# Kernel tuning notes

Hardware: AMD Instinct MI355X
Metric: run time of the kernel (lower is better)

## Reference

```python
import jax, jax.numpy as jnp
import numpy as np

C = 512  # channels
B, S = 8, 2048


def setup_inputs() -> dict:
    key = jax.random.key(0)
    ks = jax.random.split(key, 8)
    x = jax.random.normal(ks[0], (B, S, C), dtype=jnp.float32)
    eigenvalues = jax.random.normal(ks[1], (B, S), dtype=jnp.float32)
    init = 1.0 / np.sqrt(C)
    Wq = jax.random.normal(ks[2], (C, C), dtype=jnp.float32) * init
    bq = jnp.zeros((C,), dtype=jnp.float32)
    Wk = jax.random.normal(ks[3], (C, C), dtype=jnp.float32) * init
    bk = jnp.zeros((C,), dtype=jnp.float32)
    Wv = jax.random.normal(ks[4], (C, C), dtype=jnp.float32) * init
    bv = jnp.zeros((C,), dtype=jnp.float32)
    return {"x": x, "eigenvalues": eigenvalues, "Wq": Wq, "bq": bq,
            "Wk": Wk, "bk": bk, "Wv": Wv, "bv": bv}


def reference(x, eigenvalues, Wq, bq, Wk, bk, Wv, bv):
    # torch nn.Linear: y = x @ W^T + b
    scale = 1.0 / np.sqrt(x.shape[-1])
    Q = jnp.einsum('bsc,dc->bsd', x, Wq) + bq
    K = jnp.einsum('bsc,dc->bsd', x, Wk) + bk
    V = jnp.einsum('bsc,dc->bsd', x, Wv) + bv
    # scores: [B, S(query), S(key)]
    scores = jnp.einsum('bqd,bkd->bqk', Q, K) * scale
    eigen_weight = jax.nn.sigmoid(eigenvalues)          # [B, S]
    scores = scores * eigen_weight[:, None, :]          # scale per key position
    attn = jax.nn.softmax(scores, axis=-1)
    return jnp.einsum('bqk,bkd->bqd', attn, V)
```

## Files before the change

kernel.cpp:

```cpp
#include <hip/hip_runtime.h>

typedef unsigned short u16;
using bf16x8 = __attribute__((ext_vector_type(8))) short;
using f32x4  = __attribute__((ext_vector_type(4))) float;

__device__ __forceinline__ u16 f2b(float f) {
    __bf16 h = (__bf16)f;
    return __builtin_bit_cast(unsigned short, h);
}
__device__ __forceinline__ float b2f(u16 u) {
    return (float)__builtin_bit_cast(__bf16, u);
}

__device__ __forceinline__ void gload16(const void* g, void* l) {
    __builtin_amdgcn_global_load_lds(
        (const __attribute__((address_space(1))) unsigned int*)g,
        (__attribute__((address_space(3))) unsigned int*)l, 16, 0, 0);
}

template<int MODE>
__global__ __launch_bounds__(256)
void gemm_bt(const u16* __restrict__ A, const u16* __restrict__ B,
             void* __restrict__ Cv, const float* __restrict__ aux,
             float* __restrict__ rowsum,
             int K, int lda, int ldb, int ldc,
             long strA, long strB, long strC, long strAux, long strRS)
{
    __shared__ __align__(16) u16 sA[128 * 64];
    __shared__ __align__(16) u16 sB[128 * 64];

    const int tid  = threadIdx.x;
    const int lane = tid & 63;
    const int wave = tid >> 6;
    const int wm = wave >> 1, wn = wave & 1;
    const int bn0 = blockIdx.x * 128;
    const int bm0 = blockIdx.y * 128;
    const long z  = blockIdx.z;

    const u16* Ab = A + z * strA;
    const u16* Bb = B + z * strB;
    const float* auxp = aux + z * strAux;

    f32x4 acc[4][4] = {};

    const int l16 = lane & 15;
    const int lk8 = (lane >> 4) * 8;

    for (int k0 = 0; k0 < K; k0 += 64) {
#pragma unroll
        for (int i = 0; i < 4; ++i) {
            const int c   = i * 256 + tid;
            const int row = c >> 3;
            const int kc  = (c & 7) ^ (row & 7);
            const int ldsoff = (i * 256 + wave * 64) * 8;
            gload16(Ab + (long)(bm0 + row) * lda + k0 + kc * 8, &sA[ldsoff]);
            gload16(Bb + (long)(bn0 + row) * ldb + k0 + kc * 8, &sB[ldsoff]);
        }
        __syncthreads();
#pragma unroll
        for (int kk = 0; kk < 64; kk += 32) {
            bf16x8 af[4], bg[4];
#pragma unroll
            for (int m = 0; m < 4; ++m) {
                const int row = wm * 64 + m * 16 + l16;
                int byte_off = row * 128 + (kk + lk8) * 2;
                byte_off ^= (row & 7) << 4;
                af[m] = *(const bf16x8*)((const char*)sA + byte_off);
            }
#pragma unroll
            for (int n = 0; n < 4; ++n) {
                const int row = wn * 64 + n * 16 + l16;
                int byte_off = row * 128 + (kk + lk8) * 2;
                byte_off ^= (row & 7) << 4;
                bg[n] = *(const bf16x8*)((const char*)sB + byte_off);
            }
#pragma unroll
            for (int m = 0; m < 4; ++m)
#pragma unroll
                for (int n = 0; n < 4; ++n)
                    acc[m][n] = __builtin_amdgcn_mfma_f32_16x16x32_bf16(
                        af[m], bg[n], acc[m][n], 0, 0, 0);
        }
        __syncthreads();
    }

    const int rg    = lane >> 4;
    const int orow0 = bm0 + wm * 64;
    const int ocol0 = bn0 + wn * 64;

    if constexpr (MODE == 0) {
        u16* Co = (u16*)Cv + z * strC;
        float bias[4];
#pragma unroll
        for (int n = 0; n < 4; ++n) bias[n] = auxp[ocol0 + n * 16 + l16];
#pragma unroll
        for (int m = 0; m < 4; ++m)
#pragma unroll
            for (int n = 0; n < 4; ++n) {
                const int col = ocol0 + n * 16 + l16;
#pragma unroll
                for (int r = 0; r < 4; ++r) {
                    const int row = orow0 + m * 16 + rg * 4 + r;
                    Co[(long)row * ldc + col] = f2b(acc[m][n][r] + bias[n]);
                }
            }
    } else if constexpr (MODE == 2) {
        u16* Co = (u16*)Cv + z * strC;
        float* rsp = rowsum + z * strRS;
        float wkn[4];
#pragma unroll
        for (int n = 0; n < 4; ++n) wkn[n] = auxp[ocol0 + n * 16 + l16];
#pragma unroll
        for (int m = 0; m < 4; ++m)
#pragma unroll
            for (int r = 0; r < 4; ++r) {
                const int row = orow0 + m * 16 + rg * 4 + r;
                float partial = 0.f;
#pragma unroll
                for (int n = 0; n < 4; ++n) {
                    const int col = ocol0 + n * 16 + l16;
                    const float p = exp2f(acc[m][n][r] * wkn[n]);
                    const u16 pb = f2b(p);
                    Co[(long)row * ldc + col] = pb;
                    partial += b2f(pb);
                }
                partial += __shfl_xor(partial, 1);
                partial += __shfl_xor(partial, 2);
                partial += __shfl_xor(partial, 4);
                partial += __shfl_xor(partial, 8);
                if (l16 == 0) atomicAdd(&rsp[row], partial);
            }
    } else {
        float* Co = (float*)Cv + z * strC;
#pragma unroll
        for (int m = 0; m < 4; ++m)
#pragma unroll
            for (int r = 0; r < 4; ++r) {
                const int row = orow0 + m * 16 + rg * 4 + r;
                const float inv = 1.0f / auxp[row];
#pragma unroll
                for (int n = 0; n < 4; ++n) {
                    const int col = ocol0 + n * 16 + l16;
                    Co[(long)row * ldc + col] = acc[m][n][r] * inv;
                }
            }
    }
}

__global__ void cvt_bf16(const float* __restrict__ in, u16* __restrict__ out, int n4) {
    const int i = blockIdx.x * 256 + threadIdx.x;
    if (i >= n4) return;
    const float4 f = ((const float4*)in)[i];
    ushort4 o;
    o.x = f2b(f.x); o.y = f2b(f.y); o.z = f2b(f.z); o.w = f2b(f.w);
    ((ushort4*)out)[i] = o;
}

__global__ void wk_kernel(const float* __restrict__ eig, float* __restrict__ wk, int n) {
    const int i = blockIdx.x * 256 + threadIdx.x;
    if (i >= n) return;
    const float s = 1.0f / (1.0f + expf(-eig[i]));
    wk[i] = s * (float)(1.4426950408889634 / 22.627416997969522);
}

__global__ __launch_bounds__(256)
void transpose_v(const u16* __restrict__ V, u16* __restrict__ Vt) {
    __shared__ u16 t[64][65];
    const int tid = threadIdx.x;
    const int d0  = blockIdx.x * 64;
    const int bs0 = blockIdx.y * 64;
#pragma unroll
    for (int i = 0; i < 16; ++i) {
        const int idx = i * 256 + tid;
        const int r = idx >> 6, c = idx & 63;
        t[r][c] = V[(long)(bs0 + r) * 512 + d0 + c];
    }
    __syncthreads();
    const long b = bs0 >> 11;
    const int s0 = bs0 & 2047;
#pragma unroll
    for (int i = 0; i < 16; ++i) {
        const int idx = i * 256 + tid;
        const int dch = idx >> 6, s = idx & 63;
        Vt[(b * 512 + d0 + dch) * 2048 + s0 + s] = t[s][dch];
    }
}

extern "C" void kernel_launch(void* const* d_in, const int* in_sizes, int n_in,
                              void* d_out, int out_size, void* d_ws, size_t ws_size,
                              hipStream_t stream) {
    const float* x  = (const float*)d_in[0];
    const float* ev = (const float*)d_in[1];
    const float* Wq = (const float*)d_in[2];
    const float* bq = (const float*)d_in[3];
    const float* Wk = (const float*)d_in[4];
    const float* bk = (const float*)d_in[5];
    const float* Wv = (const float*)d_in[6];
    const float* bv = (const float*)d_in[7];
    float* out = (float*)d_out;

    char* ws = (char*)d_ws;
    u16*   xb     = (u16*)(ws);
    u16*   qkv    = (u16*)(ws + (16ul << 20));
    u16*   Vt     = (u16*)(ws + (64ul << 20));
    u16*   Wb     = (u16*)(ws + (80ul << 20));
    float* biasb  = (float*)(ws + (82ul << 20));
    float* wk     = (float*)(ws + (83ul << 20));
    float* rowsum = (float*)(ws + (84ul << 20));
    u16*   P      = (u16*)(ws + (85ul << 20));

    cvt_bf16<<<dim3(8192), dim3(256), 0, stream>>>(x, xb, 2097152);
    cvt_bf16<<<dim3(256),  dim3(256), 0, stream>>>(Wq, Wb,          65536);
    cvt_bf16<<<dim3(256),  dim3(256), 0, stream>>>(Wk, Wb + 262144, 65536);
    cvt_bf16<<<dim3(256),  dim3(256), 0, stream>>>(Wv, Wb + 524288, 65536);
    hipMemcpyAsync(biasb,        bq, 512 * 4, hipMemcpyDeviceToDevice, stream);
    hipMemcpyAsync(biasb + 512,  bk, 512 * 4, hipMemcpyDeviceToDevice, stream);
    hipMemcpyAsync(biasb + 1024, bv, 512 * 4, hipMemcpyDeviceToDevice, stream);
    wk_kernel<<<dim3(64), dim3(256), 0, stream>>>(ev, wk, 16384);
    hipMemsetAsync(rowsum, 0, 16384 * 4, stream);

    gemm_bt<0><<<dim3(4, 128, 3), dim3(256), 0, stream>>>(
        xb, Wb, qkv, biasb, nullptr,
        512, 512, 512, 512,
        0L, 262144L, 8388608L, 512L, 0L);

    transpose_v<<<dim3(8, 256), dim3(256), 0, stream>>>(qkv + 2 * 8388608L, Vt);

    gemm_bt<2><<<dim3(16, 16, 8), dim3(256), 0, stream>>>(
        qkv, qkv + 8388608L, P, wk, rowsum,
        512, 512, 512, 2048,
        1048576L, 1048576L, 4194304L, 2048L, 2048L);

    gemm_bt<3><<<dim3(4, 16, 8), dim3(256), 0, stream>>>(
        P, Vt, out, rowsum, nullptr,
        2048, 2048, 2048, 512,
        4194304L, 1048576L, 1048576L, 2048L, 0L);
}
```

Measured before the change: 265.3 us.

## Rewrite GEMMs as 8-wave 256-row tiles with double-buffered LDS pipeline

Replaces the 128x128 single-buffered GEMM with an 8-wave kernel using 256-row tiles (256x128 or 256x256), split-K-half double-buffered LDS staging, and hand-placed waitcnt/barriers with setprio around MFMA bursts. It also remaps block indices for L2 locality and fuses the QKV projection into one interleaved 1536-wide output GEMM. The aim is to overlap global-to-LDS loads with MFMA work and raise data reuse per tile. The cost is more registers and LDS, fewer blocks for the PV GEMM, and fragile manual synchronisation.

```diff
diff --git a/kernel.cpp b/kernel.cpp
--- a/kernel.cpp
+++ b/kernel.cpp
@@ -11,115 +11,197 @@
 __device__ __forceinline__ float b2f(u16 u) {
     return (float)__builtin_bit_cast(__bf16, u);
 }
-
-__device__ __forceinline__ void gload16(const void* g, void* l) {
+__device__ __forceinline__ void gload16(const u16* g, const u16* l) {
     __builtin_amdgcn_global_load_lds(
         (const __attribute__((address_space(1))) unsigned int*)g,
         (__attribute__((address_space(3))) unsigned int*)l, 16, 0, 0);
 }
-
-template<int MODE>
-__global__ __launch_bounds__(256)
-void gemm_bt(const u16* __restrict__ A, const u16* __restrict__ B,
-             void* __restrict__ Cv, const float* __restrict__ aux,
-             float* __restrict__ rowsum,
-             int K, int lda, int ldb, int ldc,
-             long strA, long strB, long strC, long strAux, long strRS)
+__device__ __forceinline__ int swz(int row, int q) { return q ^ ((row ^ (row >> 2)) & 3); }
+
+template<int MODE, int NBLK>
+__global__ __launch_bounds__(512, 2)
+void gemm8(const u16* __restrict__ A, const u16* __restrict__ B,
+           void* __restrict__ Cv, const float* __restrict__ aux,
+           float* __restrict__ rowsum,
+           int K, int lda, int ldb, int ldc,
+           long strA, long strB, long strC, long strAux, long strRS)
 {
-    __shared__ __align__(16) u16 sA[128 * 64];
-    __shared__ __align__(16) u16 sB[128 * 64];
+    constexpr int BR  = NBLK * 64;
+    constexpr int VMC = (NBLK == 4) ? 6 : 5;
+    __shared__ __align__(16) u16 sA[2][2][256 * 32];
+    __shared__ __align__(16) u16 sB[2][2][BR * 32];
 
     const int tid  = threadIdx.x;
     const int lane = tid & 63;
     const int wave = tid >> 6;
-    const int wm = wave >> 1, wn = wave & 1;
-    const int bn0 = blockIdx.x * 128;
-    const int bm0 = blockIdx.y * 128;
-    const long z  = blockIdx.z;
-
-    const u16* Ab = A + z * strA;
-    const u16* Bb = B + z * strB;
+    const int wm = wave >> 2, wn = wave & 3;
+    const int l16 = lane & 15, qld = lane >> 4;
+
+    const int gx = gridDim.x, gy = gridDim.y;
+    const int nxy = gx * gy;
+    int li = blockIdx.y * gx + blockIdx.x;
+    li = (li & 7) * (nxy >> 3) + (li >> 3);
+    const int bx = li % gx, by = li / gx;
+    const int bn0 = bx * BR, bm0 = by * 256;
+    const long z = blockIdx.z;
+
+    const u16* Ab = A + z * strA + (long)bm0 * lda;
+    const u16* Bb = B + z * strB + (long)bn0 * ldb;
     const float* auxp = aux + z * strAux;
 
-    f32x4 acc[4][4] = {};
-
-    const int l16 = lane & 15;
-    const int lk8 = (lane >> 4) * 8;
-
-    for (int k0 = 0; k0 < K; k0 += 64) {
-#pragma unroll
-        for (int i = 0; i < 4; ++i) {
-            const int c   = i * 256 + tid;
-            const int row = c >> 3;
-            const int kc  = (c & 7) ^ (row & 7);
-            const int ldsoff = (i * 256 + wave * 64) * 8;
-            gload16(Ab + (long)(bm0 + row) * lda + k0 + kc * 8, &sA[ldsoff]);
-            gload16(Bb + (long)(bn0 + row) * ldb + k0 + kc * 8, &sB[ldsoff]);
-        }
-        __syncthreads();
-#pragma unroll
-        for (int kk = 0; kk < 64; kk += 32) {
-            bf16x8 af[4], bg[4];
-#pragma unroll
-            for (int m = 0; m < 4; ++m) {
-                const int row = wm * 64 + m * 16 + l16;
-                int byte_off = row * 128 + (kk + lk8) * 2;
-                byte_off ^= (row & 7) << 4;
-                af[m] = *(const bf16x8*)((const char*)sA + byte_off);
-            }
-#pragma unroll
-            for (int n = 0; n < 4; ++n) {
-                const int row = wn * 64 + n * 16 + l16;
-                int byte_off = row * 128 + (kk + lk8) * 2;
-                byte_off ^= (row & 7) << 4;
-                bg[n] = *(const bf16x8*)((const char*)sB + byte_off);
-            }
-#pragma unroll
-            for (int m = 0; m < 4; ++m)
-#pragma unroll
-                for (int n = 0; n < 4; ++n)
-                    acc[m][n] = __builtin_amdgcn_mfma_f32_16x16x32_bf16(
-                        af[m], bg[n], acc[m][n], 0, 0, 0);
-        }
-        __syncthreads();
-    }
-
-    const int rg    = lane >> 4;
-    const int orow0 = bm0 + wm * 64;
-    const int ocol0 = bn0 + wn * 64;
+    const int cA0 = tid, cA1 = 512 + tid;
+    const u16* srcA0 = Ab + (long)(cA0 >> 2) * lda + swz(cA0 >> 2, cA0 & 3) * 8;
+    const u16* srcA1 = Ab + (long)(cA1 >> 2) * lda + swz(cA1 >> 2, cA1 & 3) * 8;
+    const int cB1 = (NBLK == 4) ? cA1 : cA0;
+    const u16* srcB0 = Bb + (long)(cA0 >> 2) * ldb + swz(cA0 >> 2, cA0 & 3) * 8;
+    const u16* srcB1 = Bb + (long)(cB1 >> 2) * ldb + swz(cB1 >> 2, cB1 & 3) * 8;
+    const int wch = (tid & ~63) * 8;
+
+#define STAGE_A(sl, kh, colb) do { \
+    gload16(srcA0 + (colb), &sA[sl][kh][wch]); \
+    gload16(srcA1 + (colb), &sA[sl][kh][wch + 4096]); } while (0)
+#define STAGE_B(sl, kh, colb) do { \
+    gload16(srcB0 + (colb), &sB[sl][kh][wch]); \
+    if constexpr (NBLK == 4) { gload16(srcB1 + (colb), &sB[sl][kh][wch + 4096]); } } while (0)
+
+    int offA[8], offB[NBLK];
+#pragma unroll
+    for (int mf = 0; mf < 8; ++mf) {
+        const int row = wm * 128 + mf * 16 + l16;
+        offA[mf] = row * 32 + swz(row, qld) * 8;
+    }
+#pragma unroll
+    for (int n = 0; n < NBLK; ++n) {
+        const int row = wn * (NBLK * 16) + n * 16 + l16;
+        offB[n] = row * 32 + swz(row, qld) * 8;
+    }
+
+    f32x4 acc[8][NBLK] = {};
+    const int NT = K >> 6;
+
+    STAGE_A(0, 0, 0);
+    STAGE_B(0, 0, 0);
+    STAGE_A(0, 1, 32);
+    STAGE_B(0, 1, 32);
+    if (NT > 1) STAGE_A(1, 0, 64);
+    asm volatile("s_waitcnt vmcnt(2)" ::: "memory");
+    __builtin_amdgcn_sched_barrier(0);
+    asm volatile("s_barrier" ::: "memory");
+
+    for (int t = 0; t < NT; ++t) {
+        const int s = t & 1, s1 = s ^ 1;
+        const int kc1 = (t + 1) << 6;
+        const bool i1 = (t + 1 < NT), i2 = (t + 2 < NT);
+        const bool tail = (t >= NT - 2);
+
+        bf16x8 afr[4], bfr[NBLK];
+#pragma unroll
+        for (int j = 0; j < 4; ++j) afr[j] = *(const bf16x8*)&sA[s][0][offA[j]];
+#pragma unroll
+        for (int n = 0; n < NBLK; ++n) bfr[n] = *(const bf16x8*)&sB[s][0][offB[n]];
+        if (i1) STAGE_B(s1, 0, kc1);
+        asm volatile("s_barrier" ::: "memory");
+        __builtin_amdgcn_s_setprio(1);
+#pragma unroll
+        for (int j = 0; j < 4; ++j)
+#pragma unroll
+            for (int n = 0; n < NBLK; ++n)
+                acc[j][n] = __builtin_amdgcn_mfma_f32_16x16x32_bf16(afr[j], bfr[n], acc[j][n], 0, 0, 0);
+        __builtin_amdgcn_s_setprio(0);
+        asm volatile("s_waitcnt lgkmcnt(0)" ::: "memory");
+        __builtin_amdgcn_sched_barrier(0);
+        asm volatile("s_barrier" ::: "memory");
+
+#pragma unroll
+        for (int j = 0; j < 4; ++j) afr[j] = *(const bf16x8*)&sA[s][0][offA[4 + j]];
+        if (i1) STAGE_A(s1, 1, kc1 + 32);
+        asm volatile("s_barrier" ::: "memory");
+        __builtin_amdgcn_s_setprio(1);
+#pragma unroll
+        for (int j = 0; j < 4; ++j)
+#pragma unroll
+            for (int n = 0; n < NBLK; ++n)
+                acc[4 + j][n] = __builtin_amdgcn_mfma_f32_16x16x32_bf16(afr[j], bfr[n], acc[4 + j][n], 0, 0, 0);
+        __builtin_amdgcn_s_setprio(0);
+        if (tail) asm volatile("s_waitcnt vmcnt(0)" ::: "memory");
+        else      asm volatile("s_waitcnt vmcnt(%0)" :: "i"(VMC) : "memory");
+        asm volatile("s_waitcnt lgkmcnt(0)" ::: "memory");
+        __builtin_amdgcn_sched_barrier(0);
+        asm volatile("s_barrier" ::: "memory");
+
+#pragma unroll
+        for (int j = 0; j < 4; ++j) afr[j] = *(const bf16x8*)&sA[s][1][offA[j]];
+#pragma unroll
+        for (int n = 0; n < NBLK; ++n) bfr[n] = *(const bf16x8*)&sB[s][1][offB[n]];
+        if (i1) STAGE_B(s1, 1, kc1 + 32);
+        asm volatile("s_barrier" ::: "memory");
+        __builtin_amdgcn_s_setprio(1);
+#pragma unroll
+        for (int j = 0; j < 4; ++j)
+#pragma unroll
+            for (int n = 0; n < NBLK; ++n)
+                acc[j][n] = __builtin_amdgcn_mfma_f32_16x16x32_bf16(afr[j], bfr[n], acc[j][n], 0, 0, 0);
+        __builtin_amdgcn_s_setprio(0);
+        asm volatile("s_waitcnt lgkmcnt(0)" ::: "memory");
+        __builtin_amdgcn_sched_barrier(0);
+        asm volatile("s_barrier" ::: "memory");
+
+#pragma unroll
+        for (int j = 0; j < 4; ++j) afr[j] = *(const bf16x8*)&sA[s][1][offA[4 + j]];
+        if (i2) STAGE_A(s, 0, kc1 + 64);
+        asm volatile("s_barrier" ::: "memory");
+        __builtin_amdgcn_s_setprio(1);
+#pragma unroll
+        for (int j = 0; j < 4; ++j)
+#pragma unroll
+            for (int n = 0; n < NBLK; ++n)
+                acc[4 + j][n] = __builtin_amdgcn_mfma_f32_16x16x32_bf16(afr[j], bfr[n], acc[4 + j][n], 0, 0, 0);
+        __builtin_amdgcn_s_setprio(0);
+        if (tail) asm volatile("s_waitcnt vmcnt(0)" ::: "memory");
+        else      asm volatile("s_waitcnt vmcnt(%0)" :: "i"(VMC) : "memory");
+        asm volatile("s_waitcnt lgkmcnt(0)" ::: "memory");
+        __builtin_amdgcn_sched_barrier(0);
+        asm volatile("s_barrier" ::: "memory");
+    }
+#undef STAGE_A
+#undef STAGE_B
+
+    const int rg = lane >> 4;
+    const int orow0 = bm0 + wm * 128;
+    const int ocol0 = bn0 + wn * (NBLK * 16);
 
     if constexpr (MODE == 0) {
         u16* Co = (u16*)Cv + z * strC;
-        float bias[4];
-#pragma unroll
-        for (int n = 0; n < 4; ++n) bias[n] = auxp[ocol0 + n * 16 + l16];
-#pragma unroll
-        for (int m = 0; m < 4; ++m)
-#pragma unroll
-            for (int n = 0; n < 4; ++n) {
+        float bias[NBLK];
+#pragma unroll
+        for (int n = 0; n < NBLK; ++n) bias[n] = auxp[ocol0 + n * 16 + l16];
+#pragma unroll
+        for (int mf = 0; mf < 8; ++mf)
+#pragma unroll
+            for (int n = 0; n < NBLK; ++n) {
                 const int col = ocol0 + n * 16 + l16;
 #pragma unroll
                 for (int r = 0; r < 4; ++r) {
-                    const int row = orow0 + m * 16 + rg * 4 + r;
-                    Co[(long)row * ldc + col] = f2b(acc[m][n][r] + bias[n]);
+                    const int row = orow0 + mf * 16 + rg * 4 + r;
+                    Co[(long)row * ldc + col] = f2b(acc[mf][n][r] + bias[n]);
                 }
             }
     } else if constexpr (MODE == 2) {
         u16* Co = (u16*)Cv + z * strC;
         float* rsp = rowsum + z * strRS;
-        float wkn[4];
-#pragma unroll
-        for (int n = 0; n < 4; ++n) wkn[n] = auxp[ocol0 + n * 16 + l16];
-#pragma unroll
-        for (int m = 0; m < 4; ++m)
+        float wkn[NBLK];
+#pragma unroll
+        for (int n = 0; n < NBLK; ++n) wkn[n] = auxp[ocol0 + n * 16 + l16];
+#pragma unroll
+        for (int mf = 0; mf < 8; ++mf)
 #pragma unroll
             for (int r = 0; r < 4; ++r) {
-                const int row = orow0 + m * 16 + rg * 4 + r;
+                const int row = orow0 + mf * 16 + rg * 4 + r;
                 float partial = 0.f;
 #pragma unroll
-                for (int n = 0; n < 4; ++n) {
+                for (int n = 0; n < NBLK; ++n) {
                     const int col = ocol0 + n * 16 + l16;
-                    const float p = exp2f(acc[m][n][r] * wkn[n]);
+                    const float p = exp2f(acc[mf][n][r] * wkn[n]);
                     const u16 pb = f2b(p);
                     Co[(long)row * ldc + col] = pb;
                     partial += b2f(pb);
@@ -133,15 +215,15 @@
     } else {
         float* Co = (float*)Cv + z * strC;
 #pragma unroll
-        for (int m = 0; m < 4; ++m)
+        for (int mf = 0; mf < 8; ++mf)
 #pragma unroll
             for (int r = 0; r < 4; ++r) {
-                const int row = orow0 + m * 16 + rg * 4 + r;
+                const int row = orow0 + mf * 16 + rg * 4 + r;
                 const float inv = 1.0f / auxp[row];
 #pragma unroll
-                for (int n = 0; n < 4; ++n) {
+                for (int n = 0; n < NBLK; ++n) {
                     const int col = ocol0 + n * 16 + l16;
-                    Co[(long)row * ldc + col] = acc[m][n][r] * inv;
+                    Co[(long)row * ldc + col] = acc[mf][n][r] * inv;
                 }
             }
     }
@@ -164,7 +246,7 @@
 }
 
 __global__ __launch_bounds__(256)
-void transpose_v(const u16* __restrict__ V, u16* __restrict__ Vt) {
+void transpose_v(const u16* __restrict__ Vq, u16* __restrict__ Vt) {
     __shared__ u16 t[64][65];
     const int tid = threadIdx.x;
     const int d0  = blockIdx.x * 64;
@@ -173,7 +255,7 @@
     for (int i = 0; i < 16; ++i) {
         const int idx = i * 256 + tid;
         const int r = idx >> 6, c = idx & 63;
-        t[r][c] = V[(long)(bs0 + r) * 512 + d0 + c];
+        t[r][c] = Vq[(long)(bs0 + r) * 1536 + d0 + c];
     }
     __syncthreads();
     const long b = bs0 >> 11;
@@ -181,8 +263,8 @@
 #pragma unroll
     for (int i = 0; i < 16; ++i) {
         const int idx = i * 256 + tid;
-        const int dch = idx >> 6, s = idx & 63;
-        Vt[(b * 512 + d0 + dch) * 2048 + s0 + s] = t[s][dch];
+        const int dch = idx >> 6, ss = idx & 63;
+        Vt[(b * 512 + d0 + dch) * 2048 + s0 + ss] = t[ss][dch];
     }
 }
 
@@ -200,14 +282,14 @@
     float* out = (float*)d_out;
 
     char* ws = (char*)d_ws;
-    u16*   xb     = (u16*)(ws);
-    u16*   qkv    = (u16*)(ws + (16ul << 20));
-    u16*   Vt     = (u16*)(ws + (64ul << 20));
-    u16*   Wb     = (u16*)(ws + (80ul << 20));
-    float* biasb  = (float*)(ws + (82ul << 20));
-    float* wk     = (float*)(ws + (83ul << 20));
-    float* rowsum = (float*)(ws + (84ul << 20));
-    u16*   P      = (u16*)(ws + (85ul << 20));
+    u16*   P      = (u16*)(ws);
+    u16*   xb     = (u16*)(ws + (64ul << 20));
+    u16*   qkvC   = (u16*)(ws + (80ul << 20));
+    u16*   Vt     = (u16*)(ws + (128ul << 20));
+    u16*   Wb     = (u16*)(ws + (144ul << 20));
+    float* biasb  = (float*)(ws + (146ul << 20));
+    float* wk     = (float*)(ws + (146ul << 20) + 65536);
+    float* rowsum = (float*)(ws + (146ul << 20) + 131072);
 
     cvt_bf16<<<dim3(8192), dim3(256), 0, stream>>>(x, xb, 2097152);
     cvt_bf16<<<dim3(256),  dim3(256), 0, stream>>>(Wq, Wb,          65536);
@@ -217,21 +299,21 @@
     hipMemcpyAsync(biasb + 512,  bk, 512 * 4, hipMemcpyDeviceToDevice, stream);
     hipMemcpyAsync(biasb + 1024, bv, 512 * 4, hipMemcpyDeviceToDevice, stream);
     wk_kernel<<<dim3(64), dim3(256), 0, stream>>>(ev, wk, 16384);
-    hipMemsetAsync(rowsum, 0, 16384 * 4, stream);
-
-    gemm_bt<0><<<dim3(4, 128, 3), dim3(256), 0, stream>>>(
-        xb, Wb, qkv, biasb, nullptr,
-        512, 512, 512, 512,
-        0L, 262144L, 8388608L, 512L, 0L);
-
-    transpose_v<<<dim3(8, 256), dim3(256), 0, stream>>>(qkv + 2 * 8388608L, Vt);
-
-    gemm_bt<2><<<dim3(16, 16, 8), dim3(256), 0, stream>>>(
-        qkv, qkv + 8388608L, P, wk, rowsum,
-        512, 512, 512, 2048,
-        1048576L, 1048576L, 4194304L, 2048L, 2048L);
-
-    gemm_bt<3><<<dim3(4, 16, 8), dim3(256), 0, stream>>>(
+    hipMemsetAsync(rowsum, 0, 65536, stream);
+
+    gemm8<0, 2><<<dim3(12, 64, 1), dim3(512), 0, stream>>>(
+        xb, Wb, qkvC, biasb, nullptr,
+        512, 512, 512, 1536,
+        0L, 0L, 0L, 0L, 0L);
+
+    transpose_v<<<dim3(8, 256), dim3(256), 0, stream>>>(qkvC + 1024, Vt);
+
+    gemm8<2, 4><<<dim3(8, 8, 8), dim3(512), 0, stream>>>(
+        qkvC, qkvC + 512, P, wk, rowsum,
+        512, 1536, 1536, 2048,
+        3145728L, 3145728L, 4194304L, 2048L, 2048L);
+
+    gemm8<3, 2><<<dim3(4, 8, 8), dim3(512), 0, stream>>>(
         P, Vt, out, rowsum, nullptr,
         2048, 2048, 2048, 512,
         4194304L, 1048576L, 1048576L, 2048L, 0L);
```

After: 269.5 us. Within noise of the previous version (+1.6%).
